# Optimization experiments

Measured on AMD Instinct MI355X. Metric: run time of the kernel, lower is better.

## Reference

```python
import jax, jax.numpy as jnp
from jax import lax
import numpy as np

H = 51  # hidden size hardcoded in the torch module


def _lstm_cell(x, h, c, W_ih, W_hh, b):
    # torch LSTMCell: gates = x @ W_ih.T + h @ W_hh.T + (b_ih + b_hh); order i,f,g,o
    gates = x @ W_ih.T + h @ W_hh.T + b
    i, f, g, o = jnp.split(gates, 4, axis=-1)
    c_new = jax.nn.sigmoid(f) * c + jax.nn.sigmoid(i) * jnp.tanh(g)
    h_new = jax.nn.sigmoid(o) * jnp.tanh(c_new)
    return h_new, c_new


def setup_inputs() -> dict:
    key = jax.random.key(0)
    ks = jax.random.split(key, 16)
    B, T = 1024, 512
    s = 1.0 / np.sqrt(H)
    u = lambda k, shape: jax.random.uniform(k, shape, jnp.float32, -s, s)
    inp = {
        'input': jax.random.normal(ks[0], (B, T), jnp.float32),
        'W_ih1': u(ks[1], (4 * H, 1)),
        'W_hh1': u(ks[2], (4 * H, H)),
        'b_ih1': u(ks[3], (4 * H,)),
        'b_hh1': u(ks[4], (4 * H,)),
        'W_ih2': u(ks[5], (4 * H, H)),
        'W_hh2': u(ks[6], (4 * H, H)),
        'b_ih2': u(ks[7], (4 * H,)),
        'b_hh2': u(ks[8], (4 * H,)),
        'W_ih3': u(ks[9], (4 * H, H)),
        'W_hh3': u(ks[10], (4 * H, H)),
        'b_ih3': u(ks[11], (4 * H,)),
        'b_hh3': u(ks[12], (4 * H,)),
        'W_lin': u(ks[13], (1, H)),
        'b_lin': u(ks[14], (1,)),
        'future': 64,
    }
    return inp


def reference(input, W_ih1, W_hh1, b_ih1, b_hh1,
              W_ih2, W_hh2, b_ih2, b_hh2,
              W_ih3, W_hh3, b_ih3, b_hh3,
              W_lin, b_lin, future):
    B = input.shape[0]
    b1 = b_ih1 + b_hh1
    b2 = b_ih2 + b_hh2
    b3 = b_ih3 + b_hh3
    z = jnp.zeros((B, H), input.dtype)
    carry0 = (z, z, z, z, z, z)

    def stack_step(carry, x_t):
        h1, c1, h2, c2, h3, c3 = carry
        h1, c1 = _lstm_cell(x_t, h1, c1, W_ih1, W_hh1, b1)
        h2, c2 = _lstm_cell(h1, h2, c2, W_ih2, W_hh2, b2)
        h3, c3 = _lstm_cell(h2, h3, c3, W_ih3, W_hh3, b3)
        out = h3 @ W_lin.T + b_lin  # [B, 1]
        return (h1, c1, h2, c2, h3, c3), out

    xs = input.T[:, :, None]  # [T, B, 1]
    carry, outs = lax.scan(stack_step, carry0, xs)  # outs: [T, B, 1]

    if future > 0:
        def future_step(fcarry, _):
            carry, out = fcarry
            carry, out = stack_step(carry, out)
            return (carry, out), out

        _, fouts = lax.scan(future_step, (carry, outs[-1]), None, length=future)
        outs = jnp.concatenate([outs, fouts], axis=0)  # [T+future, B, 1]

    return jnp.transpose(outs, (1, 0, 2))[:, :, 0]  # [B, T+future]
```

## Files before the change

kernel.cpp:

```cpp
#include <hip/hip_runtime.h>

#define H      51
#define T_IN   512
#define T_TOT  576
#define PH     56
#define NR     204
#define LDSB   (5 * NR * PH * 2)

typedef _Float16 h2v __attribute__((ext_vector_type(2)));

__device__ __forceinline__ float bf2f(unsigned short u) {
    return __uint_as_float(((unsigned int)u) << 16);
}
__device__ __forceinline__ unsigned short f2bf(float f) {
    unsigned int u = __float_as_uint(f);
    u += 0x7fffu + ((u >> 16) & 1u);
    return (unsigned short)(u >> 16);
}
__device__ __forceinline__ float wget(const void* p, int i, bool is16) {
    return is16 ? bf2f(((const unsigned short*)p)[i]) : ((const float*)p)[i];
}
__device__ __forceinline__ float sigm(float x) {
    x = fminf(fmaxf(x, -30.f), 30.f);
    return 1.f / (1.f + __expf(-x));
}
__device__ __forceinline__ float tanh_f(float x) {
    x = fminf(fmaxf(x, -15.f), 15.f);
    float e = __expf(2.f * x);
    return (e - 1.f) / (e + 1.f);
}
__device__ __forceinline__ h2v bch2(unsigned int u) {
    return __builtin_bit_cast(h2v, u);
}
__device__ __forceinline__ h2v rlh2(h2v v, int m) {
    unsigned int r = (unsigned int)__builtin_amdgcn_readlane(
        (int)__builtin_bit_cast(unsigned int, v), m);
    return __builtin_bit_cast(h2v, r);
}
__device__ __forceinline__ h2v pkh2(float a, float b) {
    return __builtin_bit_cast(h2v, __builtin_amdgcn_cvt_pkrtz(a, b));
}
#if __has_builtin(__builtin_amdgcn_fdot2)
__device__ __forceinline__ float dot2(unsigned int w, h2v s, float acc) {
    return __builtin_amdgcn_fdot2(bch2(w), s, acc, false);
}
#else
__device__ __forceinline__ float dot2(unsigned int w, h2v s, float acc) {
    h2v wv = bch2(w);
    acc = fmaf((float)wv.x, (float)s.x, acc);
    return fmaf((float)wv.y, (float)s.y, acc);
}
#endif
#define SBAR() __builtin_amdgcn_sched_barrier(0)

extern "C" __global__ void __launch_bounds__(256)
__attribute__((amdgpu_waves_per_eu(2, 2)))
lstm3_kernel(const void* g_in,  const void* g_Wih1, const void* g_Whh1,
             const void* g_bih1, const void* g_bhh1,
             const void* g_Wih2, const void* g_Whh2, const void* g_bih2, const void* g_bhh2,
             const void* g_Wih3, const void* g_Whh3, const void* g_bih3, const void* g_bhh3,
             const void* g_Wlin, const void* g_blin, void* g_out)
{
    extern __shared__ char smraw[];
    _Float16* W1h = (_Float16*)smraw;
    _Float16* W2i = W1h + NR * PH;
    _Float16* W2h = W2i + NR * PH;
    _Float16* W3i = W2h + NR * PH;
    _Float16* W3h = W3i + NR * PH;

    const int tid  = threadIdx.x;
    const int lane = tid & 63;
    const int wid  = tid >> 6;
    const int e    = blockIdx.x * 4 + wid;
    const int jeff = (lane < H) ? lane : (H - 1);

    bool is16 = true;
    {
        const unsigned short* p = (const unsigned short*)g_Wih1;
        for (int i = 0; i < 204; ++i) {
            float v = fabsf(bf2f(p[i]));
            if (!(v < 0.2f)) is16 = false;
        }
    }

    for (int i = tid; i < NR * PH; i += 256) {
        int r = i / PH, k = i - r * PH;
        bool v = (k < H);
        W1h[i] = v ? (_Float16)wget(g_Whh1, r * H + k, is16) : (_Float16)0.f;
        W2i[i] = v ? (_Float16)wget(g_Wih2, r * H + k, is16) : (_Float16)0.f;
        W2h[i] = v ? (_Float16)wget(g_Whh2, r * H + k, is16) : (_Float16)0.f;
        W3i[i] = v ? (_Float16)wget(g_Wih3, r * H + k, is16) : (_Float16)0.f;
        W3h[i] = v ? (_Float16)wget(g_Whh3, r * H + k, is16) : (_Float16)0.f;
    }
    __syncthreads();

    const float b1_0 = wget(g_bih1, 0*H+jeff, is16) + wget(g_bhh1, 0*H+jeff, is16);
    const float b1_1 = wget(g_bih1, 1*H+jeff, is16) + wget(g_bhh1, 1*H+jeff, is16);
    const float b1_2 = wget(g_bih1, 2*H+jeff, is16) + wget(g_bhh1, 2*H+jeff, is16);
    const float b1_3 = wget(g_bih1, 3*H+jeff, is16) + wget(g_bhh1, 3*H+jeff, is16);
    const float b2_0 = wget(g_bih2, 0*H+jeff, is16) + wget(g_bhh2, 0*H+jeff, is16);
    const float b2_1 = wget(g_bih2, 1*H+jeff, is16) + wget(g_bhh2, 1*H+jeff, is16);
    const float b2_2 = wget(g_bih2, 2*H+jeff, is16) + wget(g_bhh2, 2*H+jeff, is16);
    const float b2_3 = wget(g_bih2, 3*H+jeff, is16) + wget(g_bhh2, 3*H+jeff, is16);
    const float b3_0 = wget(g_bih3, 0*H+jeff, is16) + wget(g_bhh3, 0*H+jeff, is16);
    const float b3_1 = wget(g_bih3, 1*H+jeff, is16) + wget(g_bhh3, 1*H+jeff, is16);
    const float b3_2 = wget(g_bih3, 2*H+jeff, is16) + wget(g_bhh3, 2*H+jeff, is16);
    const float b3_3 = wget(g_bih3, 3*H+jeff, is16) + wget(g_bhh3, 3*H+jeff, is16);
    const float wi1_0 = wget(g_Wih1, 0*H+jeff, is16);
    const float wi1_1 = wget(g_Wih1, 1*H+jeff, is16);
    const float wi1_2 = wget(g_Wih1, 2*H+jeff, is16);
    const float wi1_3 = wget(g_Wih1, 3*H+jeff, is16);
    const float wlin  = (lane < H) ? wget(g_Wlin, lane, is16) : 0.f;
    const float blin  = wget(g_blin, 0, is16);

    const _Float16* R1  = W1h + jeff * PH;
    const _Float16* R2i = W2i + jeff * PH;
    const _Float16* R2h = W2h + jeff * PH;
    const _Float16* R3i = W3i + jeff * PH;
    const _Float16* R3h = W3h + jeff * PH;
#define U4(base, g, kb)  (*(const uint4*)((base) + (g) * 51 * PH + (kb) * 8))

    float h1 = 0.f, h2 = 0.f, h3 = 0.f;
    float c1 = 0.f, c2 = 0.f, c3 = 0.f;
    h2v hp1 = bch2(0u), hp2 = bch2(0u), hp3 = bch2(0u);
    float xf = 0.f;

    const unsigned short* in16 = (const unsigned short*)g_in;
    const float*          in32 = (const float*)g_in;
    unsigned short* o16 = (unsigned short*)g_out + (size_t)e * T_TOT;
    float*          o32 = (float*)g_out + (size_t)e * T_TOT;

    float xn = is16 ? bf2f(in16[(size_t)e * T_IN]) : in32[(size_t)e * T_IN];

#define ACT(cm, hv) { \
    float i_ = sigm(a0), f_ = sigm(a1), g_ = tanh_f(a2), o_ = sigm(a3); \
    cm = f_ * cm + i_ * g_; \
    hv = o_ * tanh_f(cm); }

#define PACKH(hv, hp) { \
    float he_ = __shfl(hv, 2*lane, 64); \
    float ho_ = __shfl(hv, 2*lane + 1, 64); \
    hp = pkh2(he_, ho_); }

#define DOTBLK(base, hp, kb) { \
    uint4 u0 = U4(base, 0, kb), u1 = U4(base, 1, kb); \
    uint4 u2 = U4(base, 2, kb), u3 = U4(base, 3, kb); \
    h2v s0 = rlh2(hp, 4*(kb)+0), s1 = rlh2(hp, 4*(kb)+1); \
    h2v s2 = rlh2(hp, 4*(kb)+2), s3 = rlh2(hp, 4*(kb)+3); \
    a0 = dot2(u0.x, s0, a0); a0 = dot2(u0.y, s1, a0); \
    a0 = dot2(u0.z, s2, a0); a0 = dot2(u0.w, s3, a0); \
    a1 = dot2(u1.x, s0, a1); a1 = dot2(u1.y, s1, a1); \
    a1 = dot2(u1.z, s2, a1); a1 = dot2(u1.w, s3, a1); \
    a2 = dot2(u2.x, s0, a2); a2 = dot2(u2.y, s1, a2); \
    a2 = dot2(u2.z, s2, a2); a2 = dot2(u2.w, s3, a2); \
    a3 = dot2(u3.x, s0, a3); a3 = dot2(u3.y, s1, a3); \
    a3 = dot2(u3.z, s2, a3); a3 = dot2(u3.w, s3, a3); }

#pragma clang loop unroll(disable)
    for (int t = 0; t < T_TOT; ++t) {
        float x = (t < T_IN) ? xn : xf;
        if (t + 1 < T_IN)
            xn = is16 ? bf2f(in16[(size_t)e * T_IN + t + 1])
                      : in32[(size_t)e * T_IN + t + 1];

        if (lane < H) {
            float a0 = fmaf(wi1_0, x, b1_0);
            float a1 = fmaf(wi1_1, x, b1_1);
            float a2 = fmaf(wi1_2, x, b1_2);
            float a3 = fmaf(wi1_3, x, b1_3);
#pragma unroll
            for (int kb = 0; kb < 7; ++kb) {
                DOTBLK(R1, hp1, kb)
            }
            ACT(c1, h1)
            PACKH(h1, hp1)
            SBAR();

            a0 = b2_0; a1 = b2_1; a2 = b2_2; a3 = b2_3;
#pragma unroll
            for (int kb = 0; kb < 7; ++kb) {
                DOTBLK(R2i, hp1, kb)
                DOTBLK(R2h, hp2, kb)
            }
            ACT(c2, h2)
            PACKH(h2, hp2)
            SBAR();

            a0 = b3_0; a1 = b3_1; a2 = b3_2; a3 = b3_3;
#pragma unroll
            for (int kb = 0; kb < 7; ++kb) {
                DOTBLK(R3i, hp2, kb)
                DOTBLK(R3h, hp3, kb)
            }
            ACT(c3, h3)
            PACKH(h3, hp3)
        }

        float hp = wlin * h3;
        hp += __shfl_xor(hp, 1, 64);  hp += __shfl_xor(hp, 2, 64);
        hp += __shfl_xor(hp, 4, 64);  hp += __shfl_xor(hp, 8, 64);
        hp += __shfl_xor(hp, 16, 64); hp += __shfl_xor(hp, 32, 64);
        float ov = hp + blin;
        xf = ov;
        if (lane == 0) {
            if (is16) o16[t] = f2bf(ov);
            else      o32[t] = ov;
        }
    }
}

extern "C" void kernel_launch(void* const* d_in, const int* in_sizes, int n_in,
                              void* d_out, int out_size, void* d_ws, size_t ws_size,
                              hipStream_t stream) {
    (void)in_sizes; (void)n_in; (void)d_ws; (void)ws_size; (void)out_size;
    size_t shmem = LDSB;
    hipFuncSetAttribute((const void*)lstm3_kernel,
                        hipFuncAttributeMaxDynamicSharedMemorySize, (int)shmem);
    lstm3_kernel<<<dim3(256), dim3(256), shmem, stream>>>(
        d_in[0],  d_in[1],  d_in[2],  d_in[3],  d_in[4],
        d_in[5],  d_in[6],  d_in[7],  d_in[8],
        d_in[9],  d_in[10], d_in[11], d_in[12],
        d_in[13], d_in[14], d_out);
}
```

Baseline: 1.893 ms.

## Broadcast hidden state via LDS instead of readlane, defer output head reduction

Replaces the shuffle-pack plus per-element readlane broadcast of hidden states with each lane writing its fp16 h value to a per-wave LDS buffer, which the dot products then read as 16-byte vector loads. The output linear-head reduction for the teacher-forced steps is moved to the start of the next iteration so it can overlap with the next step's work. The split into separate input and future loops removes a per-step branch. The sigmoid clamp is also dropped. The change relies on wave-synchronous LDS write-then-read visibility within a single wave, and it adds LDS traffic and latency in exchange for fewer SALU/readlane operations.

```diff
diff --git a/kernel.cpp b/kernel.cpp
--- a/kernel.cpp
+++ b/kernel.cpp
@@ -5,7 +5,9 @@
 #define T_TOT  576
 #define PH     56
 #define NR     204
-#define LDSB   (5 * NR * PH * 2)
+#define HBW    64
+#define HBOFF  (5 * NR * PH)
+#define LDSB   ((HBOFF + 4 * 3 * HBW) * 2)
 
 typedef _Float16 h2v __attribute__((ext_vector_type(2)));
 
@@ -21,7 +23,6 @@
     return is16 ? bf2f(((const unsigned short*)p)[i]) : ((const float*)p)[i];
 }
 __device__ __forceinline__ float sigm(float x) {
-    x = fminf(fmaxf(x, -30.f), 30.f);
     return 1.f / (1.f + __expf(-x));
 }
 __device__ __forceinline__ float tanh_f(float x) {
@@ -31,14 +32,6 @@
 }
 __device__ __forceinline__ h2v bch2(unsigned int u) {
     return __builtin_bit_cast(h2v, u);
-}
-__device__ __forceinline__ h2v rlh2(h2v v, int m) {
-    unsigned int r = (unsigned int)__builtin_amdgcn_readlane(
-        (int)__builtin_bit_cast(unsigned int, v), m);
-    return __builtin_bit_cast(h2v, r);
-}
-__device__ __forceinline__ h2v pkh2(float a, float b) {
-    return __builtin_bit_cast(h2v, __builtin_amdgcn_cvt_pkrtz(a, b));
 }
 #if __has_builtin(__builtin_amdgcn_fdot2)
 __device__ __forceinline__ float dot2(unsigned int w, h2v s, float acc) {
@@ -67,6 +60,7 @@
     _Float16* W2h = W2i + NR * PH;
     _Float16* W3i = W2h + NR * PH;
     _Float16* W3h = W3i + NR * PH;
+    _Float16* HBA = (_Float16*)smraw + HBOFF;
 
     const int tid  = threadIdx.x;
     const int lane = tid & 63;
@@ -92,7 +86,12 @@
         W3i[i] = v ? (_Float16)wget(g_Wih3, r * H + k, is16) : (_Float16)0.f;
         W3h[i] = v ? (_Float16)wget(g_Whh3, r * H + k, is16) : (_Float16)0.f;
     }
+    for (int i = tid; i < 4 * 3 * HBW; i += 256) HBA[i] = (_Float16)0.f;
     __syncthreads();
+
+    _Float16* hb1 = HBA + wid * (3 * HBW);
+    _Float16* hb2 = hb1 + HBW;
+    _Float16* hb3 = hb2 + HBW;
 
     const float b1_0 = wget(g_bih1, 0*H+jeff, is16) + wget(g_bhh1, 0*H+jeff, is16);
     const float b1_1 = wget(g_bih1, 1*H+jeff, is16) + wget(g_bhh1, 1*H+jeff, is16);
@@ -119,10 +118,10 @@
     const _Float16* R3i = W3i + jeff * PH;
     const _Float16* R3h = W3h + jeff * PH;
 #define U4(base, g, kb)  (*(const uint4*)((base) + (g) * 51 * PH + (kb) * 8))
+#define HV4(hb, kb)      (*(const uint4*)((const char*)(hb) + 16 * (kb)))
 
     float h1 = 0.f, h2 = 0.f, h3 = 0.f;
     float c1 = 0.f, c2 = 0.f, c3 = 0.f;
-    h2v hp1 = bch2(0u), hp2 = bch2(0u), hp3 = bch2(0u);
     float xf = 0.f;
 
     const unsigned short* in16 = (const unsigned short*)g_in;
@@ -137,16 +136,13 @@
     cm = f_ * cm + i_ * g_; \
     hv = o_ * tanh_f(cm); }
 
-#define PACKH(hv, hp) { \
-    float he_ = __shfl(hv, 2*lane, 64); \
-    float ho_ = __shfl(hv, 2*lane + 1, 64); \
-    hp = pkh2(he_, ho_); }
-
-#define DOTBLK(base, hp, kb) { \
+#define PUBH(hv, hb) { (hb)[jeff] = (_Float16)(hv); }
+
+#define DOTBLK(base, hb, kb) { \
     uint4 u0 = U4(base, 0, kb), u1 = U4(base, 1, kb); \
     uint4 u2 = U4(base, 2, kb), u3 = U4(base, 3, kb); \
-    h2v s0 = rlh2(hp, 4*(kb)+0), s1 = rlh2(hp, 4*(kb)+1); \
-    h2v s2 = rlh2(hp, 4*(kb)+2), s3 = rlh2(hp, 4*(kb)+3); \
+    uint4 hv = HV4(hb, kb); \
+    h2v s0 = bch2(hv.x), s1 = bch2(hv.y), s2 = bch2(hv.z), s3 = bch2(hv.w); \
     a0 = dot2(u0.x, s0, a0); a0 = dot2(u0.y, s1, a0); \
     a0 = dot2(u0.z, s2, a0); a0 = dot2(u0.w, s3, a0); \
     a1 = dot2(u1.x, s0, a1); a1 = dot2(u1.y, s1, a1); \
@@ -156,56 +152,70 @@
     a3 = dot2(u3.x, s0, a3); a3 = dot2(u3.y, s1, a3); \
     a3 = dot2(u3.z, s2, a3); a3 = dot2(u3.w, s3, a3); }
 
+#define STEPBODY(xv) { \
+    if (lane < H) { \
+        float a0 = fmaf(wi1_0, (xv), b1_0); \
+        float a1 = fmaf(wi1_1, (xv), b1_1); \
+        float a2 = fmaf(wi1_2, (xv), b1_2); \
+        float a3 = fmaf(wi1_3, (xv), b1_3); \
+        _Pragma("unroll") \
+        for (int kb = 0; kb < 7; ++kb) { DOTBLK(R1, hb1, kb) } \
+        ACT(c1, h1) \
+        PUBH(h1, hb1) \
+        SBAR(); \
+        a0 = b2_0; a1 = b2_1; a2 = b2_2; a3 = b2_3; \
+        _Pragma("unroll") \
+        for (int kb = 0; kb < 7; ++kb) { \
+            DOTBLK(R2i, hb1, kb) \
+            DOTBLK(R2h, hb2, kb) \
+        } \
+        ACT(c2, h2) \
+        PUBH(h2, hb2) \
+        SBAR(); \
+        a0 = b3_0; a1 = b3_1; a2 = b3_2; a3 = b3_3; \
+        _Pragma("unroll") \
+        for (int kb = 0; kb < 7; ++kb) { \
+            DOTBLK(R3i, hb2, kb) \
+            DOTBLK(R3h, hb3, kb) \
+        } \
+        ACT(c3, h3) \
+        PUBH(h3, hb3) \
+    } }
+
+#define HEADRED(res) { \
+    float hp_ = wlin * h3; \
+    hp_ += __shfl_xor(hp_, 1, 64);  hp_ += __shfl_xor(hp_, 2, 64); \
+    hp_ += __shfl_xor(hp_, 4, 64);  hp_ += __shfl_xor(hp_, 8, 64); \
+    hp_ += __shfl_xor(hp_, 16, 64); hp_ += __shfl_xor(hp_, 32, 64); \
+    res = hp_ + blin; }
+
+#define STORE(ti, ov) { if (lane == 0) { \
+    if (is16) o16[ti] = f2bf(ov); else o32[ti] = (ov); } }
+
 #pragma clang loop unroll(disable)
-    for (int t = 0; t < T_TOT; ++t) {
-        float x = (t < T_IN) ? xn : xf;
+    for (int t = 0; t < T_IN; ++t) {
+        if (t > 0) {
+            float ov; HEADRED(ov)
+            STORE(t - 1, ov)
+        }
+        float x = xn;
         if (t + 1 < T_IN)
             xn = is16 ? bf2f(in16[(size_t)e * T_IN + t + 1])
                       : in32[(size_t)e * T_IN + t + 1];
-
-        if (lane < H) {
-            float a0 = fmaf(wi1_0, x, b1_0);
-            float a1 = fmaf(wi1_1, x, b1_1);
-            float a2 = fmaf(wi1_2, x, b1_2);
-            float a3 = fmaf(wi1_3, x, b1_3);
-#pragma unroll
-            for (int kb = 0; kb < 7; ++kb) {
-                DOTBLK(R1, hp1, kb)
-            }
-            ACT(c1, h1)
-            PACKH(h1, hp1)
-            SBAR();
-
-            a0 = b2_0; a1 = b2_1; a2 = b2_2; a3 = b2_3;
-#pragma unroll
-            for (int kb = 0; kb < 7; ++kb) {
-                DOTBLK(R2i, hp1, kb)
-                DOTBLK(R2h, hp2, kb)
-            }
-            ACT(c2, h2)
-            PACKH(h2, hp2)
-            SBAR();
-
-            a0 = b3_0; a1 = b3_1; a2 = b3_2; a3 = b3_3;
-#pragma unroll
-            for (int kb = 0; kb < 7; ++kb) {
-                DOTBLK(R3i, hp2, kb)
-                DOTBLK(R3h, hp3, kb)
-            }
-            ACT(c3, h3)
-            PACKH(h3, hp3)
-        }
-
-        float hp = wlin * h3;
-        hp += __shfl_xor(hp, 1, 64);  hp += __shfl_xor(hp, 2, 64);
-        hp += __shfl_xor(hp, 4, 64);  hp += __shfl_xor(hp, 8, 64);
-        hp += __shfl_xor(hp, 16, 64); hp += __shfl_xor(hp, 32, 64);
-        float ov = hp + blin;
+        STEPBODY(x)
+    }
+    {
+        float ov; HEADRED(ov)
+        STORE(T_IN - 1, ov)
         xf = ov;
-        if (lane == 0) {
-            if (is16) o16[t] = f2bf(ov);
-            else      o32[t] = ov;
-        }
+    }
+
+#pragma clang loop unroll(disable)
+    for (int t = T_IN; t < T_TOT; ++t) {
+        STEPBODY(xf)
+        float ov; HEADRED(ov)
+        STORE(t, ov)
+        xf = ov;
     }
 }
 
```

Measured after the change: 1.817 ms. -4.0%, faster.
